# Optimization experiments

Measured on AMD Instinct MI355X. Metric: run time of the kernel, lower is better.

Reference implementation:

```python
import jax, jax.numpy as jnp
import numpy as np

DIM = 768
HEAD_DIM = 768


def setup_inputs() -> dict:
    key = jax.random.key(0)
    k_x, k_w, k_b = jax.random.split(key, 3)
    x = jax.random.normal(k_x, (4, 4096, DIM), dtype=jnp.float32)
    # torch Linear(dim, 3*head_dim): weight [3H, dim]; store transposed [dim, 3H]
    scale = 1.0 / np.sqrt(DIM)
    W_qkv = jax.random.uniform(k_w, (DIM, 3 * HEAD_DIM), dtype=jnp.float32,
                               minval=-scale, maxval=scale)
    b_qkv = jax.random.uniform(k_b, (3 * HEAD_DIM,), dtype=jnp.float32,
                               minval=-scale, maxval=scale)
    return {"x": x, "W_qkv": W_qkv, "b_qkv": b_qkv}


def reference(x, W_qkv, b_qkv):
    # x: [B, N, C]
    qkv = jnp.einsum("bnc,ch->bnh", x, W_qkv) + b_qkv  # [B, N, 3H]
    q, k, v = jnp.split(qkv, 3, axis=-1)               # each [B, N, H]
    H = q.shape[-1]
    scores = jnp.einsum("bnh,bmh->bnm", q, k) / jnp.sqrt(jnp.float32(H))
    attn = jax.nn.softmax(scores, axis=-1)             # [B, N, N]
    out = jnp.einsum("bnm,bmh->bnh", attn, v)          # [B, N, H]
    return out
```

## Files before the change

kernel.cpp:

```cpp
#include <hip/hip_runtime.h>
#include <stdint.h>

typedef __attribute__((ext_vector_type(8))) short short8;
typedef __attribute__((ext_vector_type(4))) float f32x4;

#define DIM 768
#define H3 2304
#define SEQ 4096
#define NTOK 16384
#define EP_LD 136

__device__ __forceinline__ unsigned short f2bf(float f) {
  union { float f; uint32_t u; } c; c.f = f;
  uint32_t u = c.u;
  u += 0x7FFFu + ((u >> 16) & 1u);
  return (unsigned short)(u >> 16);
}

__device__ __forceinline__ void async_cp16(const void* g, void* l) {
  __builtin_amdgcn_global_load_lds(
      (__attribute__((address_space(1))) void*)(void*)g,
      (__attribute__((address_space(3))) void*)l, 16, 0, 0);
}

__device__ __forceinline__ void gemm_nt64(
    const unsigned short* __restrict__ A, const unsigned short* __restrict__ B,
    int K, int ldA, int ldB,
    unsigned short* As, unsigned short* Bs, f32x4 acc[4][4])
{
  const int tid = threadIdx.x, lane = tid & 63, wid = tid >> 6;
  const int wm = (wid & 1) << 6, wn = (wid >> 1) << 6;
  const int lr = lane & 15, q = lane >> 4;

#pragma unroll
  for (int i = 0; i < 4; ++i)
#pragma unroll
    for (int j = 0; j < 4; ++j)
      acc[i][j] = (f32x4){0.f, 0.f, 0.f, 0.f};

  const unsigned short* gA[4];
  const unsigned short* gB[4];
#pragma unroll
  for (int t = 0; t < 4; ++t) {
    const int c = tid + 256 * t;
    const int row = c >> 3, sc = c & 7;
    const int col8 = ((sc ^ (row & 7)) << 3);
    gA[t] = A + (size_t)row * ldA + col8;
    gB[t] = B + (size_t)row * ldB + col8;
  }

  for (int k0 = 0; k0 < K; k0 += 64) {
#pragma unroll
    for (int t = 0; t < 4; ++t)
      async_cp16(gA[t] + k0, As + (tid + 256 * t) * 8);
#pragma unroll
    for (int t = 0; t < 4; ++t)
      async_cp16(gB[t] + k0, Bs + (tid + 256 * t) * 8);
    __syncthreads();

    short8 af[4][2], bfr[4][2];
#pragma unroll
    for (int i = 0; i < 4; ++i) {
      const int ra = wm + i * 16 + lr;
#pragma unroll
      for (int s2 = 0; s2 < 2; ++s2)
        af[i][s2] = *(const short8*)(As + ra * 64 + (((s2 * 4 + q) ^ (ra & 7)) << 3));
    }
#pragma unroll
    for (int j = 0; j < 4; ++j) {
      const int rb = wn + j * 16 + lr;
#pragma unroll
      for (int s2 = 0; s2 < 2; ++s2)
        bfr[j][s2] = *(const short8*)(Bs + rb * 64 + (((s2 * 4 + q) ^ (rb & 7)) << 3));
    }
#pragma unroll
    for (int s2 = 0; s2 < 2; ++s2)
#pragma unroll
      for (int i = 0; i < 4; ++i)
#pragma unroll
        for (int j = 0; j < 4; ++j)
          acc[i][j] = __builtin_amdgcn_mfma_f32_16x16x32_bf16(af[i][s2], bfr[j][s2], acc[i][j], 0, 0, 0);
    __syncthreads();
  }
}

__global__ __launch_bounds__(256) void k_cvt(const float* __restrict__ in,
                                             unsigned short* __restrict__ o) {
  int i = blockIdx.x * 256 + threadIdx.x;
  float4 f = ((const float4*)in)[i];
  ushort4 u;
  u.x = f2bf(f.x); u.y = f2bf(f.y); u.z = f2bf(f.z); u.w = f2bf(f.w);
  ((ushort4*)o)[i] = u;
}

__global__ __launch_bounds__(256) void k_transpose(const float* __restrict__ W,
                                                   unsigned short* __restrict__ Wt) {
  __shared__ float tile[32][33];
  const int bc = blockIdx.x * 32;
  const int br = blockIdx.y * 32;
  const int tx = threadIdx.x & 31, ty = threadIdx.x >> 5;
#pragma unroll
  for (int i = 0; i < 32; i += 8)
    tile[ty + i][tx] = W[(size_t)(br + ty + i) * H3 + bc + tx];
  __syncthreads();
#pragma unroll
  for (int i = 0; i < 32; i += 8)
    Wt[(size_t)(bc + ty + i) * DIM + br + tx] = f2bf(tile[tx][ty + i]);
}

__global__ __launch_bounds__(256) void k_qkv(
    const unsigned short* __restrict__ xbf, const unsigned short* __restrict__ Wt,
    const float* __restrict__ bias,
    unsigned short* __restrict__ qb, unsigned short* __restrict__ kb,
    unsigned short* __restrict__ vT)
{
  __shared__ unsigned short As[128 * 64];
  __shared__ unsigned short Bs[128 * 64];
  f32x4 acc[4][4];
  const int g = blockIdx.x;
  const int xcd = g & 7, slot = g >> 3;
  const int tn = slot % 18, grp = slot / 18;
  const int tm = xcd + 8 * grp;
  gemm_nt64(xbf + (size_t)(tm * 128) * DIM, Wt + (size_t)(tn * 128) * DIM,
            DIM, DIM, DIM, As, Bs, acc);

  const int tid = threadIdx.x, lane = tid & 63, wid = tid >> 6;
  const int wm = (wid & 1) << 6, wn = (wid >> 1) << 6;
  const float scale = 0.036084391824351615f;
#pragma unroll
  for (int i = 0; i < 4; ++i) {
#pragma unroll
    for (int j = 0; j < 4; ++j) {
      const int col  = tn * 128 + wn + j * 16 + (lane & 15);
      const int row0 = tm * 128 + wm + i * 16 + ((lane >> 4) << 2);
      const float bc = bias[col];
#pragma unroll
      for (int r = 0; r < 4; ++r) {
        const int row = row0 + r;
        const float v = acc[i][j][r] + bc;
        if (col < 768) {
          qb[(size_t)row * DIM + col] = f2bf(v * scale);
        } else if (col < 1536) {
          kb[(size_t)row * DIM + (col - 768)] = f2bf(v);
        } else {
          const int b = row >> 12, n = row & 4095;
          vT[((size_t)b * DIM + (col - 1536)) * SEQ + n] = f2bf(v);
        }
      }
    }
  }
}

__global__ __launch_bounds__(256) void k_scores(
    const unsigned short* __restrict__ qb, const unsigned short* __restrict__ kb,
    unsigned short* __restrict__ S, float* __restrict__ lpart)
{
  __shared__ unsigned short sm[128 * EP_LD];
  unsigned short* As = sm;
  unsigned short* Bs = sm + 128 * 64;
  f32x4 acc[4][4];
  const int g = blockIdx.x;
  const int xcd = g & 7, slot = g >> 3;
  const int tn = slot & 31, grp = slot >> 5;
  const int s  = xcd + 8 * grp;
  const int ty = s & 31, b = s >> 5;
  const unsigned short* A  = qb + (size_t)b * SEQ * DIM + (size_t)(ty * 128) * DIM;
  const unsigned short* Bm = kb + (size_t)b * SEQ * DIM + (size_t)(tn * 128) * DIM;
  unsigned short* Sb = S + (size_t)b * SEQ * SEQ;
  gemm_nt64(A, Bm, DIM, DIM, DIM, As, Bs, acc);

  const int tid = threadIdx.x, lane = tid & 63, wid = tid >> 6;
  const int wm = (wid & 1) << 6, wn = (wid >> 1) << 6;
  const int q = lane >> 4;
  float rs[4][4];
#pragma unroll
  for (int i = 0; i < 4; ++i) {
#pragma unroll
    for (int r = 0; r < 4; ++r) rs[i][r] = 0.f;
#pragma unroll
    for (int j = 0; j < 4; ++j) {
      const int col  = wn + j * 16 + (lane & 15);
      const int row0 = wm + i * 16 + (q << 2);
#pragma unroll
      for (int r = 0; r < 4; ++r) {
        const float e = __expf(acc[i][j][r]);
        sm[(row0 + r) * EP_LD + col] = f2bf(e);
        rs[i][r] += e;
      }
    }
  }
  const int half = wid >> 1;
  const int lbase = b * SEQ + ty * 128 + wm + (q << 2);
  float* lp = lpart + (size_t)(tn * 2 + half) * NTOK;
#pragma unroll
  for (int i = 0; i < 4; ++i)
#pragma unroll
    for (int r = 0; r < 4; ++r) {
      float v = rs[i][r];
      v += __shfl_xor(v, 1); v += __shfl_xor(v, 2);
      v += __shfl_xor(v, 4); v += __shfl_xor(v, 8);
      if ((lane & 15) == 0)
        lp[lbase + i * 16 + r] = v;
    }
  __syncthreads();
  const int rL = tid >> 4, cc = (tid & 15) << 3;
#pragma unroll
  for (int p = 0; p < 8; ++p) {
    const int row = p * 16 + rL;
    *(uint4*)(Sb + (size_t)(ty * 128 + row) * SEQ + tn * 128 + cc) =
        *(const uint4*)(sm + row * EP_LD + cc);
  }
}

__global__ __launch_bounds__(256) void k_lred(const float* __restrict__ lpart,
                                              float* __restrict__ lsum) {
  const int tid = threadIdx.x;
  const int row = blockIdx.x * 64 + (tid >> 2);
  const int part = tid & 3;
  float s = 0.f;
#pragma unroll
  for (int t = 0; t < 16; ++t)
    s += lpart[(size_t)(part * 16 + t) * NTOK + row];
  s += __shfl_xor(s, 1);
  s += __shfl_xor(s, 2);
  if (part == 0) lsum[row] = 1.0f / s;
}

__global__ __launch_bounds__(256) void k_pv(
    const unsigned short* __restrict__ P, const unsigned short* __restrict__ vT,
    const float* __restrict__ lsum, float* __restrict__ out)
{
  __shared__ unsigned short As[128 * 64];
  __shared__ unsigned short Bs[128 * 64];
  f32x4 acc[4][4];
  const int g = blockIdx.x;
  const int xcd = g & 7, slot = g >> 3;
  const int tn = slot % 6, grp = slot / 6;
  const int s  = xcd + 8 * grp;
  const int ty = s & 31, b = s >> 5;

  const unsigned short* A  = P  + (size_t)b * SEQ * SEQ + (size_t)(ty * 128) * SEQ;
  const unsigned short* Bm = vT + (size_t)b * DIM * SEQ + (size_t)(tn * 128) * SEQ;
  float* ob = out + (size_t)b * SEQ * DIM;
  gemm_nt64(A, Bm, SEQ, SEQ, SEQ, As, Bs, acc);

  const int tid = threadIdx.x, lane = tid & 63, wid = tid >> 6;
  const int wm = (wid & 1) << 6, wn = (wid >> 1) << 6;
  const int q = lane >> 4;
  const int lbase = b * SEQ + ty * 128 + wm + (q << 2);
  float inv[4][4];
#pragma unroll
  for (int i = 0; i < 4; ++i)
#pragma unroll
    for (int r = 0; r < 4; ++r)
      inv[i][r] = lsum[lbase + i * 16 + r];
#pragma unroll
  for (int i = 0; i < 4; ++i)
#pragma unroll
    for (int j = 0; j < 4; ++j) {
      const int col  = tn * 128 + wn + j * 16 + (lane & 15);
      const int row0 = ty * 128 + wm + i * 16 + (q << 2);
#pragma unroll
      for (int r = 0; r < 4; ++r)
        ob[(size_t)(row0 + r) * DIM + col] = acc[i][j][r] * inv[i][r];
    }
}

extern "C" void kernel_launch(void* const* d_in, const int* in_sizes, int n_in,
                              void* d_out, int out_size, void* d_ws, size_t ws_size,
                              hipStream_t stream) {
  const float* x    = (const float*)d_in[0];
  const float* W    = (const float*)d_in[1];
  const float* bias = (const float*)d_in[2];
  float* out = (float*)d_out;

  char* w = (char*)d_ws;
  unsigned short* x_bf = (unsigned short*)(w);
  unsigned short* Wt   = (unsigned short*)(w + 25165824);
  unsigned short* qb   = (unsigned short*)(w + 28704768);
  unsigned short* kb   = (unsigned short*)(w + 53870592);
  unsigned short* vT   = (unsigned short*)(w + 79036416);
  unsigned short* S    = (unsigned short*)(w + 104202240);
  float* lpart = (float*)(w);
  float* lsum  = (float*)(w + 4194304);

  k_cvt      <<<12288, 256, 0, stream>>>(x, x_bf);
  k_transpose<<<dim3(72, 24), 256, 0, stream>>>(W, Wt);
  k_qkv      <<<2304, 256, 0, stream>>>(x_bf, Wt, bias, qb, kb, vT);
  k_scores   <<<4096, 256, 0, stream>>>(qb, kb, S, lpart);
  k_lred     <<<256, 256, 0, stream>>>(lpart, lsum);
  k_pv       <<<768, 256, 0, stream>>>(S, vT, lsum, out);
}
```

Baseline: 504.8 us.

## Retile PV GEMM to 128x96, loop QKV tiles per block, swizzle scores epilogue

Templates the shared GEMM on the number of N sub-tiles so the PV kernel can use 128x96 tiles with 1024 blocks instead of 128x128 with 768. The QKV projection block now computes two adjacent N tiles sequentially, halving its grid. The scores epilogue replaces padded LDS staging with an XOR-swizzled layout to avoid bank conflicts while using less shared memory. The smaller PV tile trades per-block data reuse for better balance across CUs.

```diff
diff --git a/kernel.cpp b/kernel.cpp
--- a/kernel.cpp
+++ b/kernel.cpp
@@ -8,7 +8,6 @@
 #define H3 2304
 #define SEQ 4096
 #define NTOK 16384
-#define EP_LD 136
 
 __device__ __forceinline__ unsigned short f2bf(float f) {
   union { float f; uint32_t u; } c; c.f = f;
@@ -23,30 +22,35 @@
       (__attribute__((address_space(3))) void*)l, 16, 0, 0);
 }
 
-__device__ __forceinline__ void gemm_nt64(
+template<int JN>
+__device__ __forceinline__ void gemm_nt64_t(
     const unsigned short* __restrict__ A, const unsigned short* __restrict__ B,
     int K, int ldA, int ldB,
-    unsigned short* As, unsigned short* Bs, f32x4 acc[4][4])
+    unsigned short* As, unsigned short* Bs, f32x4 acc[4][JN])
 {
   const int tid = threadIdx.x, lane = tid & 63, wid = tid >> 6;
-  const int wm = (wid & 1) << 6, wn = (wid >> 1) << 6;
+  const int wm = (wid & 1) << 6, wn = (wid >> 1) * (JN * 16);
   const int lr = lane & 15, q = lane >> 4;
 
 #pragma unroll
   for (int i = 0; i < 4; ++i)
 #pragma unroll
-    for (int j = 0; j < 4; ++j)
+    for (int j = 0; j < JN; ++j)
       acc[i][j] = (f32x4){0.f, 0.f, 0.f, 0.f};
 
   const unsigned short* gA[4];
-  const unsigned short* gB[4];
+  const unsigned short* gB[JN];
 #pragma unroll
   for (int t = 0; t < 4; ++t) {
     const int c = tid + 256 * t;
     const int row = c >> 3, sc = c & 7;
-    const int col8 = ((sc ^ (row & 7)) << 3);
-    gA[t] = A + (size_t)row * ldA + col8;
-    gB[t] = B + (size_t)row * ldB + col8;
+    gA[t] = A + (size_t)row * ldA + (((sc ^ (row & 7)) << 3));
+  }
+#pragma unroll
+  for (int t = 0; t < JN; ++t) {
+    const int c = tid + 256 * t;
+    const int row = c >> 3, sc = c & 7;
+    gB[t] = B + (size_t)row * ldB + (((sc ^ (row & 7)) << 3));
   }
 
   for (int k0 = 0; k0 < K; k0 += 64) {
@@ -54,11 +58,11 @@
     for (int t = 0; t < 4; ++t)
       async_cp16(gA[t] + k0, As + (tid + 256 * t) * 8);
 #pragma unroll
-    for (int t = 0; t < 4; ++t)
+    for (int t = 0; t < JN; ++t)
       async_cp16(gB[t] + k0, Bs + (tid + 256 * t) * 8);
     __syncthreads();
 
-    short8 af[4][2], bfr[4][2];
+    short8 af[4][2], bfr[JN][2];
 #pragma unroll
     for (int i = 0; i < 4; ++i) {
       const int ra = wm + i * 16 + lr;
@@ -67,7 +71,7 @@
         af[i][s2] = *(const short8*)(As + ra * 64 + (((s2 * 4 + q) ^ (ra & 7)) << 3));
     }
 #pragma unroll
-    for (int j = 0; j < 4; ++j) {
+    for (int j = 0; j < JN; ++j) {
       const int rb = wn + j * 16 + lr;
 #pragma unroll
       for (int s2 = 0; s2 < 2; ++s2)
@@ -78,7 +82,7 @@
 #pragma unroll
       for (int i = 0; i < 4; ++i)
 #pragma unroll
-        for (int j = 0; j < 4; ++j)
+        for (int j = 0; j < JN; ++j)
           acc[i][j] = __builtin_amdgcn_mfma_f32_16x16x32_bf16(af[i][s2], bfr[j][s2], acc[i][j], 0, 0, 0);
     __syncthreads();
   }
@@ -119,35 +123,40 @@
   f32x4 acc[4][4];
   const int g = blockIdx.x;
   const int xcd = g & 7, slot = g >> 3;
-  const int tn = slot % 18, grp = slot / 18;
+  const int tp = slot % 9, grp = slot / 9;
   const int tm = xcd + 8 * grp;
-  gemm_nt64(xbf + (size_t)(tm * 128) * DIM, Wt + (size_t)(tn * 128) * DIM,
-            DIM, DIM, DIM, As, Bs, acc);
+  const unsigned short* Abase = xbf + (size_t)(tm * 128) * DIM;
 
   const int tid = threadIdx.x, lane = tid & 63, wid = tid >> 6;
   const int wm = (wid & 1) << 6, wn = (wid >> 1) << 6;
   const float scale = 0.036084391824351615f;
-#pragma unroll
-  for (int i = 0; i < 4; ++i) {
-#pragma unroll
-    for (int j = 0; j < 4; ++j) {
-      const int col  = tn * 128 + wn + j * 16 + (lane & 15);
-      const int row0 = tm * 128 + wm + i * 16 + ((lane >> 4) << 2);
-      const float bc = bias[col];
-#pragma unroll
-      for (int r = 0; r < 4; ++r) {
-        const int row = row0 + r;
-        const float v = acc[i][j][r] + bc;
-        if (col < 768) {
-          qb[(size_t)row * DIM + col] = f2bf(v * scale);
-        } else if (col < 1536) {
-          kb[(size_t)row * DIM + (col - 768)] = f2bf(v);
-        } else {
-          const int b = row >> 12, n = row & 4095;
-          vT[((size_t)b * DIM + (col - 1536)) * SEQ + n] = f2bf(v);
+
+  for (int t2 = 0; t2 < 2; ++t2) {
+    const int tn = tp * 2 + t2;
+    gemm_nt64_t<4>(Abase, Wt + (size_t)(tn * 128) * DIM, DIM, DIM, DIM, As, Bs, acc);
+#pragma unroll
+    for (int i = 0; i < 4; ++i) {
+#pragma unroll
+      for (int j = 0; j < 4; ++j) {
+        const int col  = tn * 128 + wn + j * 16 + (lane & 15);
+        const int row0 = tm * 128 + wm + i * 16 + ((lane >> 4) << 2);
+        const float bc = bias[col];
+#pragma unroll
+        for (int r = 0; r < 4; ++r) {
+          const int row = row0 + r;
+          const float v = acc[i][j][r] + bc;
+          if (col < 768) {
+            qb[(size_t)row * DIM + col] = f2bf(v * scale);
+          } else if (col < 1536) {
+            kb[(size_t)row * DIM + (col - 768)] = f2bf(v);
+          } else {
+            const int b = row >> 12, n = row & 4095;
+            vT[((size_t)b * DIM + (col - 1536)) * SEQ + n] = f2bf(v);
+          }
         }
       }
     }
+    __syncthreads();
   }
 }
 
@@ -155,7 +164,7 @@
     const unsigned short* __restrict__ qb, const unsigned short* __restrict__ kb,
     unsigned short* __restrict__ S, float* __restrict__ lpart)
 {
-  __shared__ unsigned short sm[128 * EP_LD];
+  __shared__ unsigned short sm[128 * 128];
   unsigned short* As = sm;
   unsigned short* Bs = sm + 128 * 64;
   f32x4 acc[4][4];
@@ -167,7 +176,7 @@
   const unsigned short* A  = qb + (size_t)b * SEQ * DIM + (size_t)(ty * 128) * DIM;
   const unsigned short* Bm = kb + (size_t)b * SEQ * DIM + (size_t)(tn * 128) * DIM;
   unsigned short* Sb = S + (size_t)b * SEQ * SEQ;
-  gemm_nt64(A, Bm, DIM, DIM, DIM, As, Bs, acc);
+  gemm_nt64_t<4>(A, Bm, DIM, DIM, DIM, As, Bs, acc);
 
   const int tid = threadIdx.x, lane = tid & 63, wid = tid >> 6;
   const int wm = (wid & 1) << 6, wn = (wid >> 1) << 6;
@@ -179,12 +188,12 @@
     for (int r = 0; r < 4; ++r) rs[i][r] = 0.f;
 #pragma unroll
     for (int j = 0; j < 4; ++j) {
-      const int col  = wn + j * 16 + (lane & 15);
-      const int row0 = wm + i * 16 + (q << 2);
+      const int col = wn + j * 16 + (lane & 15);
 #pragma unroll
       for (int r = 0; r < 4; ++r) {
+        const int row = wm + i * 16 + (q << 2) + r;
         const float e = __expf(acc[i][j][r]);
-        sm[(row0 + r) * EP_LD + col] = f2bf(e);
+        sm[row * 128 + (((col >> 3) ^ (((row >> 2) & 3) << 1)) << 3) + (col & 7)] = f2bf(e);
         rs[i][r] += e;
       }
     }
@@ -203,12 +212,13 @@
         lp[lbase + i * 16 + r] = v;
     }
   __syncthreads();
-  const int rL = tid >> 4, cc = (tid & 15) << 3;
+  const int rL = tid >> 4, cc = tid & 15;
 #pragma unroll
   for (int p = 0; p < 8; ++p) {
     const int row = p * 16 + rL;
-    *(uint4*)(Sb + (size_t)(ty * 128 + row) * SEQ + tn * 128 + cc) =
-        *(const uint4*)(sm + row * EP_LD + cc);
+    const int pos = cc ^ (((row >> 2) & 3) << 1);
+    *(uint4*)(Sb + (size_t)(ty * 128 + row) * SEQ + tn * 128 + cc * 8) =
+        *(const uint4*)(sm + row * 128 + pos * 8);
   }
 }
 
@@ -231,21 +241,21 @@
     const float* __restrict__ lsum, float* __restrict__ out)
 {
   __shared__ unsigned short As[128 * 64];
-  __shared__ unsigned short Bs[128 * 64];
-  f32x4 acc[4][4];
+  __shared__ unsigned short Bs[96 * 64];
+  f32x4 acc[4][3];
   const int g = blockIdx.x;
   const int xcd = g & 7, slot = g >> 3;
-  const int tn = slot % 6, grp = slot / 6;
+  const int tn = slot & 7, grp = slot >> 3;
   const int s  = xcd + 8 * grp;
   const int ty = s & 31, b = s >> 5;
 
   const unsigned short* A  = P  + (size_t)b * SEQ * SEQ + (size_t)(ty * 128) * SEQ;
-  const unsigned short* Bm = vT + (size_t)b * DIM * SEQ + (size_t)(tn * 128) * SEQ;
+  const unsigned short* Bm = vT + (size_t)b * DIM * SEQ + (size_t)(tn * 96) * SEQ;
   float* ob = out + (size_t)b * SEQ * DIM;
-  gemm_nt64(A, Bm, SEQ, SEQ, SEQ, As, Bs, acc);
+  gemm_nt64_t<3>(A, Bm, SEQ, SEQ, SEQ, As, Bs, acc);
 
   const int tid = threadIdx.x, lane = tid & 63, wid = tid >> 6;
-  const int wm = (wid & 1) << 6, wn = (wid >> 1) << 6;
+  const int wm = (wid & 1) << 6, wn = (wid >> 1) * 48;
   const int q = lane >> 4;
   const int lbase = b * SEQ + ty * 128 + wm + (q << 2);
   float inv[4][4];
@@ -257,8 +267,8 @@
 #pragma unroll
   for (int i = 0; i < 4; ++i)
 #pragma unroll
-    for (int j = 0; j < 4; ++j) {
-      const int col  = tn * 128 + wn + j * 16 + (lane & 15);
+    for (int j = 0; j < 3; ++j) {
+      const int col  = tn * 96 + wn + j * 16 + (lane & 15);
       const int row0 = ty * 128 + wm + i * 16 + (q << 2);
 #pragma unroll
       for (int r = 0; r < 4; ++r)
@@ -286,8 +296,8 @@
 
   k_cvt      <<<12288, 256, 0, stream>>>(x, x_bf);
   k_transpose<<<dim3(72, 24), 256, 0, stream>>>(W, Wt);
-  k_qkv      <<<2304, 256, 0, stream>>>(x_bf, Wt, bias, qb, kb, vT);
+  k_qkv      <<<1152, 256, 0, stream>>>(x_bf, Wt, bias, qb, kb, vT);
   k_scores   <<<4096, 256, 0, stream>>>(qb, kb, S, lpart);
   k_lred     <<<256, 256, 0, stream>>>(lpart, lsum);
-  k_pv       <<<768, 256, 0, stream>>>(S, vT, lsum, out);
-}
+  k_pv       <<<1024, 256, 0, stream>>>(S, vT, lsum, out);
+}
```

After: 557.1 us. 1.1x slower.
